# Optimization experiments

Hardware: AMD Instinct MI355X
Metric: run time of the kernel (lower is better)

Reference implementation:

```python
import jax, jax.numpy as jnp
import numpy as np

EPS = 1e-12  # torch F.normalize default eps

def _l2_normalize(x):
    # F.normalize(x, dim=1): x / max(||x||_2, eps), per row
    n = jnp.linalg.norm(x, axis=1, keepdims=True)
    return x / jnp.maximum(n, EPS)

def setup_inputs() -> dict:
    key = jax.random.key(0)
    ks = jax.random.split(key, 7)
    B, D = 8192, 4096
    s = 1.0 / np.sqrt(D)  # keep activations well-scaled like nn.Linear init
    return {
        "x":  jax.random.normal(ks[0], (B, D), dtype=jnp.float32),
        "W0": jax.random.normal(ks[1], (D, D), dtype=jnp.float32) * s,
        "b0": jax.random.normal(ks[2], (D,),   dtype=jnp.float32) * s,
        "W1": jax.random.normal(ks[3], (D, D), dtype=jnp.float32) * s,
        "b1": jax.random.normal(ks[4], (D,),   dtype=jnp.float32) * s,
        "W2": jax.random.normal(ks[5], (D, D), dtype=jnp.float32) * s,
        "b2": jax.random.normal(ks[6], (D,),   dtype=jnp.float32) * s,
    }

def reference(x, W0, b0, W1, b1, W2, b2):
    # per layer: out = relu(Linear(l2_normalize(x, dim=1))); collect all layer outputs
    params = [(W0, b0), (W1, b1), (W2, b2)]
    outs = []
    h = x
    for W, b in params:
        hn = _l2_normalize(h)
        # nn.Linear stores weight as [out, in]: y = hn @ W.T + b
        h = jax.nn.relu(jnp.einsum('bi,oi->bo', hn, W) + b)
        outs.append(h)
    return tuple(outs)
```

## Files before the change

kernel.cpp:

```cpp
#include <hip/hip_runtime.h>
#include <hip/hip_bf16.h>


#define NROWS 8192
#define DIM   4096

typedef __bf16 bf16x8 __attribute__((ext_vector_type(8)));
typedef float  f32x4  __attribute__((ext_vector_type(4)));

__device__ static inline short f2bf(float f) {
  __hip_bfloat16 h = __float2bfloat16(f);
  return __builtin_bit_cast(short, h);
}

#define BARRIER() do { asm volatile("" ::: "memory"); \
                       __builtin_amdgcn_s_barrier();  \
                       asm volatile("" ::: "memory"); } while (0)

__global__ __launch_bounds__(512, 2)
void gemm256_bias_relu(const short* __restrict__ A,
                       const short* __restrict__ Bw,
                       const float* __restrict__ bias,
                       float* __restrict__ C,
                       int M, int N, int K)
{
  __shared__ short lds[4][16384];

  int bid = blockIdx.x;
  const int nwg = gridDim.x;
  if ((nwg & 7) == 0) { const int cpx = nwg >> 3; bid = (bid & 7) * cpx + (bid >> 3); }
  const int nbn  = N >> 8;
  const int brow = (bid / nbn) << 8;
  const int bcol = (bid % nbn) << 8;

  const int lane = threadIdx.x & 63;
  const int wid  = threadIdx.x >> 6;
  const int wr   = wid >> 2;
  const int wc   = wid & 3;

  float bv[4];
#pragma unroll
  for (int j = 0; j < 4; ++j)
    bv[j] = bias[bcol + wc * 64 + j * 16 + (lane & 15)];

  f32x4 acc[8][4] = {};

  const size_t Kz   = (size_t)K;
  const size_t rowK = Kz * 2;
  const char*  Ag   = (const char*)A;
  const char*  Bg   = (const char*)Bw;
  char* const  ldsB = (char*)&lds[0][0];

  const size_t gAl = ((size_t)(brow + lane) * Kz + (size_t)(wid * 8)) * 2;
  const size_t gBl = ((size_t)(bcol + lane) * Kz + (size_t)(wid * 8)) * 2;
  const int ldst_base = wid * 256 * 16;

  auto stage_half = [&](int tile, int op, int h) {
    const char*  gp = op ? Bg : Ag;
    const size_t gt = (op ? gBl : gAl) + (size_t)tile * 128;
    char* lb = ldsB + ((tile & 1) * 2 + op) * 32768 + ldst_base;
#pragma unroll
    for (int s = 0; s < 2; ++s) {
      const int r = h * 128 + s * 64;
      __builtin_amdgcn_global_load_lds(
          (const __attribute__((address_space(1))) void*)(gp + gt + (size_t)r * rowK),
          (__attribute__((address_space(3))) void*)(lb + r * 16), 16, 0, 0);
    }
  };

  const int aoffb = ((lane >> 4) * 256 + wr * 128 + (lane & 15)) * 16;
  const int boffb = ((lane >> 4) * 256 + wc * 64  + (lane & 15)) * 16;

  const int NT = K >> 6;

  stage_half(0, 1, 0); stage_half(0, 1, 1);
  stage_half(0, 0, 0); stage_half(0, 0, 1);
  if (NT > 1) { stage_half(1, 1, 0); stage_half(1, 1, 1); stage_half(1, 0, 0); }
  if (NT > 1) asm volatile("s_waitcnt vmcnt(6)" ::: "memory");
  else        asm volatile("s_waitcnt vmcnt(0)" ::: "memory");
  BARRIER();

  bf16x8 aF[4][2], bF[4][2];

#define MFMA_QUAD(I0, J0)                                                    \
  _Pragma("unroll")                                                          \
  for (int i = 0; i < 4; ++i)                                                \
    _Pragma("unroll")                                                        \
    for (int j = 0; j < 2; ++j)                                              \
      _Pragma("unroll")                                                      \
      for (int ks = 0; ks < 2; ++ks)                                         \
        acc[(I0) + i][(J0) + j] = __builtin_amdgcn_mfma_f32_16x16x32_bf16(   \
            aF[i][ks], bF[(J0) + j][ks], acc[(I0) + i][(J0) + j], 0, 0, 0);

  for (int t = 0; t < NT; ++t) {
    const char* At = ldsB + ((t & 1) * 2 + 0) * 32768;
    const char* Bt = ldsB + ((t & 1) * 2 + 1) * 32768;

#pragma unroll
    for (int i = 0; i < 4; ++i)
#pragma unroll
      for (int ks = 0; ks < 2; ++ks)
        aF[i][ks] = *reinterpret_cast<const bf16x8*>(At + aoffb + ks * 16384 + i * 256);
#pragma unroll
    for (int j = 0; j < 4; ++j)
#pragma unroll
      for (int ks = 0; ks < 2; ++ks)
        bF[j][ks] = *reinterpret_cast<const bf16x8*>(Bt + boffb + ks * 16384 + j * 256);
    if (t + 1 < NT) stage_half(t + 1, 0, 1);
    BARRIER();
    asm volatile("s_waitcnt lgkmcnt(0)" ::: "memory");
    __builtin_amdgcn_s_setprio(1);
    MFMA_QUAD(0, 0)
    __builtin_amdgcn_s_setprio(0);
    BARRIER();

    if (t + 2 < NT) stage_half(t + 2, 1, 0);
    BARRIER();
    __builtin_amdgcn_s_setprio(1);
    MFMA_QUAD(0, 2)
    __builtin_amdgcn_s_setprio(0);
    BARRIER();

#pragma unroll
    for (int i = 0; i < 4; ++i)
#pragma unroll
      for (int ks = 0; ks < 2; ++ks)
        aF[i][ks] = *reinterpret_cast<const bf16x8*>(At + aoffb + ks * 16384 + (i + 4) * 256);
    if (t + 2 < NT) stage_half(t + 2, 1, 1);
    BARRIER();
    asm volatile("s_waitcnt lgkmcnt(0)" ::: "memory");
    __builtin_amdgcn_s_setprio(1);
    MFMA_QUAD(4, 0)
    __builtin_amdgcn_s_setprio(0);
    BARRIER();

    if (t + 2 < NT) stage_half(t + 2, 0, 0);
    BARRIER();
    __builtin_amdgcn_s_setprio(1);
    MFMA_QUAD(4, 2)
    __builtin_amdgcn_s_setprio(0);
    if (t >= NT - 2) asm volatile("s_waitcnt vmcnt(0)" ::: "memory");
    else             asm volatile("s_waitcnt vmcnt(6)" ::: "memory");
    BARRIER();
  }
#undef MFMA_QUAD

#pragma unroll
  for (int i = 0; i < 8; ++i) {
    const int rbase = brow + wr * 128 + i * 16 + ((lane >> 4) << 2);
#pragma unroll
    for (int j = 0; j < 4; ++j) {
      const int col = bcol + wc * 64 + j * 16 + (lane & 15);
#pragma unroll
      for (int r = 0; r < 4; ++r) {
        const float v = acc[i][j][r] + bv[j];
        C[(size_t)(rbase + r) * N + col] = v > 0.f ? v : 0.f;
      }
    }
  }
}

__global__ __launch_bounds__(256)
void rownorm_bf16(const float* __restrict__ in, short* __restrict__ out)
{
  const int row = blockIdx.x;
  const int t0  = threadIdx.x;
  const float4* inr = (const float4*)(in + (size_t)row * DIM);

  float4 v[4];
  float ss = 0.f;
#pragma unroll
  for (int t = 0; t < 4; ++t) {
    v[t] = inr[t0 + t * 256];
    ss += v[t].x * v[t].x + v[t].y * v[t].y + v[t].z * v[t].z + v[t].w * v[t].w;
  }
#pragma unroll
  for (int off = 32; off > 0; off >>= 1)
    ss += __shfl_down(ss, off, 64);

  __shared__ float wss[4];
  if ((t0 & 63) == 0) wss[t0 >> 6] = ss;
  __syncthreads();
  const float tot   = wss[0] + wss[1] + wss[2] + wss[3];
  const float scale = 1.f / fmaxf(sqrtf(tot), 1e-12f);

  short4* outr = (short4*)(out + (size_t)row * DIM);
#pragma unroll
  for (int t = 0; t < 4; ++t) {
    short4 o;
    o.x = f2bf(v[t].x * scale);
    o.y = f2bf(v[t].y * scale);
    o.z = f2bf(v[t].z * scale);
    o.w = f2bf(v[t].w * scale);
    outr[t0 + t * 256] = o;
  }
}

__global__ __launch_bounds__(256)
void cast_bf16(const float* __restrict__ in, short* __restrict__ out, int n4)
{
  int i = blockIdx.x * 256 + threadIdx.x;
  const int stride = gridDim.x * 256;
  for (; i < n4; i += stride) {
    const float4 v = ((const float4*)in)[i];
    short4 o;
    o.x = f2bf(v.x);
    o.y = f2bf(v.y);
    o.z = f2bf(v.z);
    o.w = f2bf(v.w);
    ((short4*)out)[i] = o;
  }
}

extern "C" void kernel_launch(void* const* d_in, const int* in_sizes, int n_in,
                              void* d_out, int out_size, void* d_ws, size_t ws_size,
                              hipStream_t stream) {
  const float* x = (const float*)d_in[0];
  const float* W[3]    = { (const float*)d_in[1], (const float*)d_in[3], (const float*)d_in[5] };
  const float* bias[3] = { (const float*)d_in[2], (const float*)d_in[4], (const float*)d_in[6] };
  float* out = (float*)d_out;

  short* hn = (short*)d_ws;
  short* Wb = (short*)((char*)d_ws + (size_t)NROWS * DIM * 2);

  const size_t layer_elems = (size_t)NROWS * DIM;
  const float* hin = x;

  for (int L = 0; L < 3; ++L) {
    cast_bf16<<<2048, 256, 0, stream>>>(W[L], Wb, DIM * DIM / 4);
    rownorm_bf16<<<NROWS, 256, 0, stream>>>(hin, hn);
    gemm256_bias_relu<<<(NROWS / 256) * (DIM / 256), 512, 0, stream>>>(
        hn, Wb, bias[L], out + (size_t)L * layer_elems, NROWS, DIM, DIM);
    hin = out + (size_t)L * layer_elems;
  }
}
```

Measured before the change: 957.1 us.

## Switch GEMM LDS tiles to row-major XOR-swizzled layout and regroup pipeline phases

Changes the global-to-LDS staging so each row's 128-byte K-slice is stored contiguously with an XOR swizzle on 16-byte chunks. Fragment reads use matching swizzled offsets, which is meant to reduce LDS bank conflicts and to make each lane's global loads cover contiguous row segments. The main loop is regrouped into four phases of two A-row fragments against all four B fragments. The A staging for tile t+1 is split across the first two phases, and the prefetch depth changes with adjusted vmcnt waits. The tighter staging window and the more complex swizzle indexing risk exposing more load latency.

```diff
diff --git a/kernel.cpp b/kernel.cpp
--- a/kernel.cpp
+++ b/kernel.cpp
@@ -51,99 +51,109 @@
   const char*  Bg   = (const char*)Bw;
   char* const  ldsB = (char*)&lds[0][0];
 
-  const size_t gAl = ((size_t)(brow + lane) * Kz + (size_t)(wid * 8)) * 2;
-  const size_t gBl = ((size_t)(bcol + lane) * Kz + (size_t)(wid * 8)) * 2;
-  const int ldst_base = wid * 256 * 16;
+  const int r8  = lane >> 3;
+  const int kcs = (lane & 7) ^ r8;
+  const size_t gAl = (size_t)(brow + r8) * rowK + (size_t)kcs * 16;
+  const size_t gBl = (size_t)(bcol + r8) * rowK + (size_t)kcs * 16;
 
   auto stage_half = [&](int tile, int op, int h) {
     const char*  gp = op ? Bg : Ag;
     const size_t gt = (op ? gBl : gAl) + (size_t)tile * 128;
-    char* lb = ldsB + ((tile & 1) * 2 + op) * 32768 + ldst_base;
+    char* lb = ldsB + ((tile & 1) * 2 + op) * 32768;
 #pragma unroll
     for (int s = 0; s < 2; ++s) {
-      const int r = h * 128 + s * 64;
+      const int rb = h * 128 + s * 64 + wid * 8;
       __builtin_amdgcn_global_load_lds(
-          (const __attribute__((address_space(1))) void*)(gp + gt + (size_t)r * rowK),
-          (__attribute__((address_space(3))) void*)(lb + r * 16), 16, 0, 0);
+          (const __attribute__((address_space(1))) void*)(gp + gt + (size_t)rb * rowK),
+          (__attribute__((address_space(3))) void*)(lb + rb * 128), 16, 0, 0);
     }
   };
 
-  const int aoffb = ((lane >> 4) * 256 + wr * 128 + (lane & 15)) * 16;
-  const int boffb = ((lane >> 4) * 256 + wc * 64  + (lane & 15)) * 16;
+  const int l15  = lane & 15;
+  const int xlo  = ((lane >> 4) ^ (lane & 3)) * 16;
+  const int b2   = (lane >> 2) & 1;
+  const int k64[2] = { b2 << 6, (1 - b2) << 6 };
+  const int abase = (wr * 128 + l15) * 128 + xlo;
+  const int bbase = (wc * 64  + l15) * 128 + xlo;
 
   const int NT = K >> 6;
 
+  stage_half(0, 0, 0); stage_half(0, 0, 1);
   stage_half(0, 1, 0); stage_half(0, 1, 1);
-  stage_half(0, 0, 0); stage_half(0, 0, 1);
-  if (NT > 1) { stage_half(1, 1, 0); stage_half(1, 1, 1); stage_half(1, 0, 0); }
-  if (NT > 1) asm volatile("s_waitcnt vmcnt(6)" ::: "memory");
+  if (NT > 1) { stage_half(1, 1, 0); stage_half(1, 1, 1); }
+  if (NT > 1) asm volatile("s_waitcnt vmcnt(4)" ::: "memory");
   else        asm volatile("s_waitcnt vmcnt(0)" ::: "memory");
   BARRIER();
 
-  bf16x8 aF[4][2], bF[4][2];
-
-#define MFMA_QUAD(I0, J0)                                                    \
+  bf16x8 aF[2][2], bF[4][2];
+
+#define MFMA2(I0)                                                            \
   _Pragma("unroll")                                                          \
-  for (int i = 0; i < 4; ++i)                                                \
+  for (int ii = 0; ii < 2; ++ii)                                             \
     _Pragma("unroll")                                                        \
-    for (int j = 0; j < 2; ++j)                                              \
+    for (int j = 0; j < 4; ++j)                                              \
       _Pragma("unroll")                                                      \
       for (int ks = 0; ks < 2; ++ks)                                         \
-        acc[(I0) + i][(J0) + j] = __builtin_amdgcn_mfma_f32_16x16x32_bf16(   \
-            aF[i][ks], bF[(J0) + j][ks], acc[(I0) + i][(J0) + j], 0, 0, 0);
+        acc[(I0) + ii][j] = __builtin_amdgcn_mfma_f32_16x16x32_bf16(         \
+            aF[ii][ks], bF[j][ks], acc[(I0) + ii][j], 0, 0, 0);
+
+#define LOAD_A(I0)                                                           \
+  _Pragma("unroll")                                                          \
+  for (int ii = 0; ii < 2; ++ii)                                             \
+    _Pragma("unroll")                                                        \
+    for (int ks = 0; ks < 2; ++ks)                                           \
+      aF[ii][ks] = *reinterpret_cast<const bf16x8*>(                         \
+          At + abase + ((I0) + ii) * 2048 + k64[ks]);
 
   for (int t = 0; t < NT; ++t) {
     const char* At = ldsB + ((t & 1) * 2 + 0) * 32768;
     const char* Bt = ldsB + ((t & 1) * 2 + 1) * 32768;
 
-#pragma unroll
-    for (int i = 0; i < 4; ++i)
+    LOAD_A(0)
+#pragma unroll
+    for (int j = 0; j < 4; ++j)
 #pragma unroll
       for (int ks = 0; ks < 2; ++ks)
-        aF[i][ks] = *reinterpret_cast<const bf16x8*>(At + aoffb + ks * 16384 + i * 256);
-#pragma unroll
-    for (int j = 0; j < 4; ++j)
-#pragma unroll
-      for (int ks = 0; ks < 2; ++ks)
-        bF[j][ks] = *reinterpret_cast<const bf16x8*>(Bt + boffb + ks * 16384 + j * 256);
+        bF[j][ks] = *reinterpret_cast<const bf16x8*>(Bt + bbase + j * 2048 + k64[ks]);
+    if (t + 1 < NT) stage_half(t + 1, 0, 0);
+    BARRIER();
+    asm volatile("s_waitcnt lgkmcnt(0)" ::: "memory");
+    __builtin_amdgcn_s_setprio(1);
+    MFMA2(0)
+    __builtin_amdgcn_s_setprio(0);
+    BARRIER();
+
+    LOAD_A(2)
     if (t + 1 < NT) stage_half(t + 1, 0, 1);
     BARRIER();
     asm volatile("s_waitcnt lgkmcnt(0)" ::: "memory");
     __builtin_amdgcn_s_setprio(1);
-    MFMA_QUAD(0, 0)
-    __builtin_amdgcn_s_setprio(0);
-    BARRIER();
-
+    MFMA2(2)
+    __builtin_amdgcn_s_setprio(0);
+    BARRIER();
+
+    LOAD_A(4)
     if (t + 2 < NT) stage_half(t + 2, 1, 0);
     BARRIER();
-    __builtin_amdgcn_s_setprio(1);
-    MFMA_QUAD(0, 2)
-    __builtin_amdgcn_s_setprio(0);
-    BARRIER();
-
-#pragma unroll
-    for (int i = 0; i < 4; ++i)
-#pragma unroll
-      for (int ks = 0; ks < 2; ++ks)
-        aF[i][ks] = *reinterpret_cast<const bf16x8*>(At + aoffb + ks * 16384 + (i + 4) * 256);
+    asm volatile("s_waitcnt lgkmcnt(0)" ::: "memory");
+    __builtin_amdgcn_s_setprio(1);
+    MFMA2(4)
+    __builtin_amdgcn_s_setprio(0);
+    BARRIER();
+
+    LOAD_A(6)
     if (t + 2 < NT) stage_half(t + 2, 1, 1);
     BARRIER();
     asm volatile("s_waitcnt lgkmcnt(0)" ::: "memory");
     __builtin_amdgcn_s_setprio(1);
-    MFMA_QUAD(4, 0)
-    __builtin_amdgcn_s_setprio(0);
-    BARRIER();
-
-    if (t + 2 < NT) stage_half(t + 2, 0, 0);
-    BARRIER();
-    __builtin_amdgcn_s_setprio(1);
-    MFMA_QUAD(4, 2)
+    MFMA2(6)
     __builtin_amdgcn_s_setprio(0);
     if (t >= NT - 2) asm volatile("s_waitcnt vmcnt(0)" ::: "memory");
-    else             asm volatile("s_waitcnt vmcnt(6)" ::: "memory");
-    BARRIER();
-  }
-#undef MFMA_QUAD
+    else             asm volatile("s_waitcnt vmcnt(4)" ::: "memory");
+    BARRIER();
+  }
+#undef MFMA2
+#undef LOAD_A
 
 #pragma unroll
   for (int i = 0; i < 8; ++i) {
```

Result: faster. 855.3 us (-10.6%).
